# Kernel optimization log

Hardware: AMD Instinct MI355X
Metric: run time of the kernel (lower is better)

Reference implementation:

```python
import jax, jax.numpy as jnp
import numpy as np

N, E = 50000, 1600000
IN_DIM, HID, HEADS, DH, NCLS = 1280, 256, 4, 64, 6
NEG_SLOPE = 0.2
LN_EPS = 1e-5


def setup_inputs() -> dict:
    key = jax.random.key(0)
    ks = jax.random.split(key, 24)
    p = {}
    p['x'] = jax.random.normal(ks[0], (N, IN_DIM), dtype=jnp.float32)
    p['edge_index'] = jax.random.randint(ks[1], (2, E), 0, N, dtype=jnp.int64)
    s = 0.05
    p['W_in'] = jax.random.normal(ks[2], (IN_DIM, HID), dtype=jnp.float32) * s
    p['b_in'] = jnp.zeros((HID,), jnp.float32)
    for l in range(2):
        p[f'W_gat{l}'] = jax.random.normal(ks[3 + 6 * l], (HID, HEADS * DH), dtype=jnp.float32) * s
        p[f'att_src{l}'] = jax.random.normal(ks[4 + 6 * l], (HEADS, DH), dtype=jnp.float32) * s
        p[f'att_dst{l}'] = jax.random.normal(ks[5 + 6 * l], (HEADS, DH), dtype=jnp.float32) * s
        p[f'b_gat{l}'] = jnp.zeros((HEADS * DH,), jnp.float32)
        p[f'ln_g{l}'] = jnp.ones((HID,), jnp.float32)
        p[f'ln_b{l}'] = jnp.zeros((HID,), jnp.float32)
    p['W_c1'] = jax.random.normal(ks[20], (HID, HID // 2), dtype=jnp.float32) * s
    p['b_c1'] = jnp.zeros((HID // 2,), jnp.float32)
    p['W_c2'] = jax.random.normal(ks[21], (HID // 2, NCLS), dtype=jnp.float32) * s
    p['b_c2'] = jnp.zeros((NCLS,), jnp.float32)
    return p


def _layer_norm(h, g, b):
    mu = jnp.mean(h, axis=-1, keepdims=True)
    var = jnp.mean((h - mu) ** 2, axis=-1, keepdims=True)
    return (h - mu) * jax.lax.rsqrt(var + LN_EPS) * g + b


def _gat_conv(h, src, dst, W, a_src, a_dst, bias):
    # h: [N, HID] -> per-head projections [N, H, DH]
    xh = (h @ W).reshape(N, HEADS, DH)
    al_src = jnp.sum(xh * a_src, axis=-1)  # [N, H]
    al_dst = jnp.sum(xh * a_dst, axis=-1)  # [N, H]
    e = jax.nn.leaky_relu(al_src[src] + al_dst[dst], NEG_SLOPE)  # [E', H]
    # edge softmax over incoming edges of each destination node
    m = jax.ops.segment_max(e, dst, num_segments=N)
    e = jnp.exp(e - m[dst])
    denom = jax.ops.segment_sum(e, dst, num_segments=N)
    w = e / denom[dst]  # [E', H]
    msg = xh[src] * w[:, :, None]  # [E', H, DH]
    out = jax.ops.segment_sum(msg, dst, num_segments=N)  # [N, H, DH]
    return out.reshape(N, HEADS * DH) + bias


def reference(x, edge_index, W_in, b_in, W_gat0, att_src0, att_dst0, b_gat0, ln_g0, ln_b0,
              W_gat1, att_src1, att_dst1, b_gat1, ln_g1, ln_b1, W_c1, b_c1, W_c2, b_c2):
    # add self loops (PyG GATConv default)
    loop = jnp.arange(N, dtype=edge_index.dtype)
    src = jnp.concatenate([edge_index[0], loop])
    dst = jnp.concatenate([edge_index[1], loop])

    h = jax.nn.relu(x @ W_in + b_in)

    for (Wg, asrc, adst, bg, g, b) in ((W_gat0, att_src0, att_dst0, b_gat0, ln_g0, ln_b0),
                                       (W_gat1, att_src1, att_dst1, b_gat1, ln_g1, ln_b1)):
        h_new = _gat_conv(h, src, dst, Wg, asrc, adst, bg)
        h_new = jax.nn.relu(_layer_norm(h_new, g, b))
        h = h + h_new

    logits = jax.nn.relu(h @ W_c1 + b_c1) @ W_c2 + b_c2
    return logits
```

## Files before the change

kernel.cpp:

```cpp
#include <hip/hip_runtime.h>

#define NN 50000
#define EE 1600000
#define INDIM 1280
#define HID 256
#define HEADS 4
#define DHD 64
#define NCLS 6
#define NEG 0.2f
#define LNEPS 1e-5f

typedef __attribute__((ext_vector_type(8))) short short8;
typedef __attribute__((ext_vector_type(4))) float floatx4;

__device__ __forceinline__ unsigned short f2b(float f) {
    unsigned int u = __float_as_uint(f);
    u += 0x7FFF + ((u >> 16) & 1);
    return (unsigned short)(u >> 16);
}
__device__ __forceinline__ float b2f(unsigned short b) {
    return __uint_as_float(((unsigned int)b) << 16);
}

#define WAIT_LGKM0() __builtin_amdgcn_s_waitcnt(0xC07F)

__global__ void init_cnt_kernel(int* __restrict__ cnt) {
    int n = blockIdx.x * 256 + threadIdx.x;
    if (n < NN) cnt[n] = 1;
}

__global__ void count_edges_kernel(const int* __restrict__ dst, int* __restrict__ cnt) {
    int e = blockIdx.x * 256 + threadIdx.x;
    if (e < EE) atomicAdd(&cnt[dst[e]], 1);
}

__global__ __launch_bounds__(1024) void scan1_kernel(const int* __restrict__ cnt,
                                                     int* __restrict__ scanned,
                                                     int* __restrict__ chtot, int n) {
    __shared__ int wsum[16];
    int tid = threadIdx.x, lane = tid & 63, wv = tid >> 6;
    int i = blockIdx.x * 1024 + tid;
    int s = (i < n) ? cnt[i] : 0;
#pragma unroll
    for (int off = 1; off < 64; off <<= 1) {
        int t = __shfl_up(s, off, 64);
        if (lane >= off) s += t;
    }
    if (lane == 63) wsum[wv] = s;
    __syncthreads();
    if (tid < 16) {
        int ws = wsum[tid];
#pragma unroll
        for (int off = 1; off < 16; off <<= 1) {
            int t = __shfl_up(ws, off, 16);
            if (tid >= off) ws += t;
        }
        wsum[tid] = ws;
    }
    __syncthreads();
    s += (wv > 0) ? wsum[wv - 1] : 0;
    if (i < n) scanned[i] = s;
    if (tid == 1023) chtot[blockIdx.x] = s;
}

__global__ void scan2_kernel(int* __restrict__ chtot, int nch) {
    int lane = threadIdx.x;
    int v = (lane < nch) ? chtot[lane] : 0;
#pragma unroll
    for (int off = 1; off < 64; off <<= 1) {
        int t = __shfl_up(v, off, 64);
        if (lane >= off) v += t;
    }
    if (lane < nch) chtot[lane] = v;
}

__global__ void scan3_kernel(const int* __restrict__ scanned, const int* __restrict__ chtot,
                             int* __restrict__ rowptr, int n) {
    int i = blockIdx.x * 256 + threadIdx.x;
    if (i == 0) rowptr[0] = 0;
    if (i < n) {
        int ch = i >> 10;
        rowptr[i + 1] = scanned[i] + (ch ? chtot[ch - 1] : 0);
    }
}

__global__ void copyfill_kernel(const int* __restrict__ rowptr, int* __restrict__ cursor,
                                int* __restrict__ csr) {
    int n = blockIdx.x * 256 + threadIdx.x;
    if (n < NN) {
        int p = rowptr[n];
        csr[p] = n;
        cursor[n] = p + 1;
    }
}

__global__ void scatter_edges_kernel(const int* __restrict__ src, const int* __restrict__ dst,
                                     int* __restrict__ cursor, int* __restrict__ csr) {
    int e = blockIdx.x * 256 + threadIdx.x;
    if (e < EE) {
        int d = dst[e];
        int pos = atomicAdd(&cursor[d], 1);
        csr[pos] = src[e];
    }
}

__global__ void pack_w_kernel(const float* __restrict__ W, unsigned short* __restrict__ out,
                              int K, int N) {
    int idx = blockIdx.x * 256 + threadIdx.x;
    int total = (K >> 6) * (N >> 4) * 2 * 64;
    if (idx >= total) return;
    int ln = idx & 63;
    int t = idx >> 6;
    int ks = t & 1; t >>= 1;
    int NT = N >> 4;
    int nt = t % NT, kc = t / NT;
    int n = nt * 16 + (ln & 15);
    int k = kc * 64 + ks * 32 + ((ln >> 4) << 3);
    unsigned short u[8];
#pragma unroll
    for (int j = 0; j < 8; j++) u[j] = f2b(W[(size_t)(k + j) * N + n]);
    *(int4*)&out[(size_t)idx * 8] = *(const int4*)u;
}

__global__ __launch_bounds__(256) void inproj_kernel(const float* __restrict__ Af,
                                                     const unsigned short* __restrict__ Bf,
                                                     const float* __restrict__ bias,
                                                     float* __restrict__ Cf,
                                                     unsigned short* __restrict__ Cb) {
    constexpr int KI = 20;
    __shared__ __align__(16) unsigned short Als[2][8192];
    int tid = threadIdx.x, wv = tid >> 6, ln = tid & 63;
    int m0 = blockIdx.x * 128;

    int srow[4], scol[4];
#pragma unroll
    for (int i = 0; i < 4; i++) {
        int s = tid + i * 256;
        int r = s >> 3;
        srow[i] = min(m0 + r, NN - 1);
        scol[i] = ((s & 7) ^ (r & 7)) * 8;
    }

    floatx4 acc[8][4] = {};
    short8 breg[8];
    float4 af[8];

    auto issueA = [&](int k) {
#pragma unroll
        for (int i = 0; i < 4; i++) {
            const float* p = Af + (size_t)srow[i] * INDIM + k * 64 + scol[i];
            af[i * 2] = *(const float4*)p;
            af[i * 2 + 1] = *(const float4*)(p + 4);
        }
    };
    auto issueB = [&](int k) {
#pragma unroll
        for (int nw = 0; nw < 4; nw++)
#pragma unroll
            for (int ks = 0; ks < 2; ks++)
                breg[nw * 2 + ks] = *(const short8*)(
                    Bf + ((((size_t)k * 16 + (wv * 4 + nw)) * 2 + ks) * 64 + ln) * 8);
    };
    auto writeA = [&](int k) {
        unsigned short* dst = &Als[k & 1][0];
#pragma unroll
        for (int i = 0; i < 4; i++) {
            unsigned short u[8] = {f2b(af[2 * i].x), f2b(af[2 * i].y),
                                   f2b(af[2 * i].z), f2b(af[2 * i].w),
                                   f2b(af[2 * i + 1].x), f2b(af[2 * i + 1].y),
                                   f2b(af[2 * i + 1].z), f2b(af[2 * i + 1].w)};
            *(int4*)&dst[(tid + i * 256) * 8] = *(const int4*)u;
        }
    };
    auto compute = [&](int k) {
        const unsigned short* src = &Als[k & 1][0];
#pragma unroll
        for (int ks = 0; ks < 2; ks++) {
            short8 a[8];
#pragma unroll
            for (int mt = 0; mt < 8; mt++) {
                int row = mt * 16 + (ln & 15);
                int g = ks * 4 + (ln >> 4);
                a[mt] = *(const short8*)&src[row * 64 + (g ^ (row & 7)) * 8];
            }
#pragma unroll
            for (int nw = 0; nw < 4; nw++)
#pragma unroll
                for (int mt = 0; mt < 8; mt++)
                    acc[mt][nw] = __builtin_amdgcn_mfma_f32_16x16x32_bf16(
                        a[mt], breg[nw * 2 + ks], acc[mt][nw], 0, 0, 0);
        }
    };

    issueA(0);
    writeA(0);
    issueA(1);
    issueB(0);
    WAIT_LGKM0();
    __builtin_amdgcn_s_barrier();

    for (int k = 0; k < KI; k++) {
        compute(k);
        if (k + 1 < KI) {
            issueB(k + 1);
            writeA(k + 1);
        }
        if (k + 2 < KI) issueA(k + 2);
        if (k + 1 < KI) {
            WAIT_LGKM0();
            __builtin_amdgcn_s_barrier();
        }
    }

#pragma unroll
    for (int mt = 0; mt < 8; mt++) {
#pragma unroll
        for (int nw = 0; nw < 4; nw++) {
            int col = (wv * 4 + nw) * 16 + (ln & 15);
            int rb = m0 + mt * 16 + (ln >> 4) * 4;
            float bi = bias[col];
#pragma unroll
            for (int r = 0; r < 4; r++) {
                int row = rb + r;
                if (row < NN) {
                    float v = fmaxf(acc[mt][nw][r] + bi, 0.f);
                    Cf[(size_t)row * HID + col] = v;
                    Cb[(size_t)row * HID + col] = f2b(v);
                }
            }
        }
    }
}

template <int KI, int NT, int ACT, int WB16, int PROJ, int CLS>
__global__ __launch_bounds__(256) void pgemm_kernel(const unsigned short* __restrict__ Ab,
                                                    const unsigned short* __restrict__ Bf,
                                                    const float* __restrict__ bias,
                                                    unsigned short* __restrict__ Cb,
                                                    const float* __restrict__ aps,
                                                    const float* __restrict__ apd,
                                                    float* __restrict__ als,
                                                    float* __restrict__ ald,
                                                    const float* __restrict__ W2,
                                                    const float* __restrict__ b2,
                                                    float* __restrict__ out2,
                                                    int M) {
    constexpr int NW = NT / 4;
    constexpr int K = KI * 64;
    __shared__ __align__(16) unsigned short Als[2][4096];
    int tid = threadIdx.x, wv = tid >> 6, ln = tid & 63;
    int m0 = blockIdx.x * 64;

    int srow[2], scol[2];
#pragma unroll
    for (int i = 0; i < 2; i++) {
        int s = tid + i * 256;
        int r = s >> 3;
        srow[i] = min(m0 + r, M - 1);
        scol[i] = ((s & 7) ^ (r & 7)) * 8;
    }

    floatx4 acc[4][NW] = {};
    short8 breg[2][NW * 2];
    int4 ai0[2], ai1[2];

    auto issueA = [&](int k, int4* ai) {
#pragma unroll
        for (int i = 0; i < 2; i++)
            ai[i] = *(const int4*)(Ab + (size_t)srow[i] * K + k * 64 + scol[i]);
    };
    auto issueB = [&](int k, short8* b) {
#pragma unroll
        for (int nw = 0; nw < NW; nw++)
#pragma unroll
            for (int ks = 0; ks < 2; ks++)
                b[nw * 2 + ks] = *(const short8*)(
                    Bf + ((((size_t)k * NT + (wv * NW + nw)) * 2 + ks) * 64 + ln) * 8);
    };
    auto writeA = [&](int k, const int4* ai) {
        unsigned short* dst = &Als[k & 1][0];
#pragma unroll
        for (int i = 0; i < 2; i++) *(int4*)&dst[(tid + i * 256) * 8] = ai[i];
    };
    auto compute = [&](int k, const short8* b) {
        const unsigned short* src = &Als[k & 1][0];
#pragma unroll
        for (int ks = 0; ks < 2; ks++) {
            short8 a[4];
#pragma unroll
            for (int mt = 0; mt < 4; mt++) {
                int row = mt * 16 + (ln & 15);
                int g = ks * 4 + (ln >> 4);
                a[mt] = *(const short8*)&src[row * 64 + (g ^ (row & 7)) * 8];
            }
#pragma unroll
            for (int nw = 0; nw < NW; nw++)
#pragma unroll
                for (int mt = 0; mt < 4; mt++)
                    acc[mt][nw] = __builtin_amdgcn_mfma_f32_16x16x32_bf16(
                        a[mt], b[nw * 2 + ks], acc[mt][nw], 0, 0, 0);
        }
    };

    issueA(0, ai0);
    issueB(0, breg[0]);
    writeA(0, ai0);
    WAIT_LGKM0();
    __builtin_amdgcn_s_barrier();

#pragma unroll
    for (int kk = 0; kk < KI / 2; kk++) {
        int k = kk * 2;
        issueA(k + 1, ai1);
        issueB(k + 1, breg[1]);
        compute(k, breg[0]);
        writeA(k + 1, ai1);
        WAIT_LGKM0();
        __builtin_amdgcn_s_barrier();
        if (k + 2 < KI) {
            issueA(k + 2, ai0);
            issueB(k + 2, breg[0]);
        }
        compute(k + 1, breg[1]);
        if (k + 2 < KI) {
            writeA(k + 2, ai0);
            WAIT_LGKM0();
            __builtin_amdgcn_s_barrier();
        }
    }

    constexpr int Nout = NT * 16;
    if constexpr (WB16) {
#pragma unroll
        for (int mt = 0; mt < 4; mt++) {
#pragma unroll
            for (int nw = 0; nw < NW; nw++) {
                int col = (wv * NW + nw) * 16 + (ln & 15);
                int rb = m0 + mt * 16 + (ln >> 4) * 4;
                float bi = bias ? bias[col] : 0.f;
#pragma unroll
                for (int r = 0; r < 4; r++) {
                    int row = rb + r;
                    if (row < M) {
                        float v = acc[mt][nw][r] + bi;
                        if (ACT) v = fmaxf(v, 0.f);
                        Cb[(size_t)row * Nout + col] = f2b(v);
                    }
                }
            }
        }
    }

    if constexpr (PROJ) {
        float avs[NW], avd[NW];
#pragma unroll
        for (int nw = 0; nw < NW; nw++) {
            int d = nw * 16 + (ln & 15);
            avs[nw] = aps[wv * DHD + d];
            avd[nw] = apd[wv * DHD + d];
        }
#pragma unroll
        for (int mt = 0; mt < 4; mt++) {
#pragma unroll
            for (int r = 0; r < 4; r++) {
                float ssum = 0.f, dsum = 0.f;
#pragma unroll
                for (int nw = 0; nw < NW; nw++) {
                    float v = acc[mt][nw][r];
                    ssum = fmaf(v, avs[nw], ssum);
                    dsum = fmaf(v, avd[nw], dsum);
                }
#pragma unroll
                for (int m = 8; m > 0; m >>= 1) {
                    ssum += __shfl_xor(ssum, m, 16);
                    dsum += __shfl_xor(dsum, m, 16);
                }
                int row = m0 + mt * 16 + (ln >> 4) * 4 + r;
                if ((ln & 15) == 0 && row < M) {
                    als[row * 4 + wv] = ssum;
                    ald[row * 4 + wv] = dsum;
                }
            }
        }
    }

    if constexpr (CLS) {
        __shared__ float cred[64][4][NCLS];
        float w2[NW][NCLS];
#pragma unroll
        for (int nw = 0; nw < NW; nw++) {
            int col = (wv * NW + nw) * 16 + (ln & 15);
#pragma unroll
            for (int c = 0; c < NCLS; c++) w2[nw][c] = W2[col * NCLS + c];
        }
#pragma unroll
        for (int mt = 0; mt < 4; mt++) {
#pragma unroll
            for (int r = 0; r < 4; r++) {
                float p[NCLS] = {};
#pragma unroll
                for (int nw = 0; nw < NW; nw++) {
                    int col = (wv * NW + nw) * 16 + (ln & 15);
                    float v = fmaxf(acc[mt][nw][r] + bias[col], 0.f);
#pragma unroll
                    for (int c = 0; c < NCLS; c++) p[c] = fmaf(v, w2[nw][c], p[c]);
                }
#pragma unroll
                for (int m = 8; m > 0; m >>= 1)
#pragma unroll
                    for (int c = 0; c < NCLS; c++) p[c] += __shfl_xor(p[c], m, 16);
                int rl = mt * 16 + (ln >> 4) * 4 + r;
                if ((ln & 15) == 0)
#pragma unroll
                    for (int c = 0; c < NCLS; c++) cred[rl][wv][c] = p[c];
            }
        }
        __syncthreads();
        for (int t = tid; t < 64 * NCLS; t += 256) {
            int row = t / NCLS, c = t % NCLS;
            if (m0 + row < M) {
                float s = cred[row][0][c] + cred[row][1][c] + cred[row][2][c] +
                          cred[row][3][c] + b2[c];
                out2[(size_t)(m0 + row) * NCLS + c] = s;
            }
        }
    }
}

__global__ __launch_bounds__(256) void agg_ln_kernel(const int* __restrict__ rowptr,
                                                     const int* __restrict__ csr,
                                                     const float* __restrict__ al_s,
                                                     const float* __restrict__ al_d,
                                                     const unsigned short* __restrict__ xhb,
                                                     const float* __restrict__ bgat,
                                                     const float* __restrict__ g,
                                                     const float* __restrict__ bb,
                                                     float* __restrict__ h,
                                                     unsigned short* __restrict__ hb) {
    int wv = threadIdx.x >> 6, ln = threadIdx.x & 63;
    int n = blockIdx.x * 4 + wv;
    if (n >= NN) return;
    int start = rowptr[n], end = rowptr[n + 1];
    int half = ln >> 5;
    int j = ln & 31;
    int head = j >> 3;
    float adh = al_d[n * 4 + head];

    float p[8] = {}, q[8] = {};
    float dsp = 0.f, dsq = 0.f;

    int i = start + half;
    for (; i + 2 < end; i += 4) {
        int s0 = csr[i], s1 = csr[i + 2];
        float e0 = al_s[s0 * 4 + head] + adh; e0 = e0 > 0.f ? e0 : NEG * e0;
        float e1 = al_s[s1 * 4 + head] + adh; e1 = e1 > 0.f ? e1 : NEG * e1;
        float w0 = __expf(e0), w1 = __expf(e1);
        dsp += w0; dsq += w1;
        short8 u0 = *(const short8*)&xhb[(size_t)s0 * HID + j * 8];
        short8 u1 = *(const short8*)&xhb[(size_t)s1 * HID + j * 8];
#pragma unroll
        for (int k = 0; k < 8; k++) {
            p[k] = fmaf(w0, b2f((unsigned short)u0[k]), p[k]);
            q[k] = fmaf(w1, b2f((unsigned short)u1[k]), q[k]);
        }
    }
    if (i < end) {
        int s0 = csr[i];
        float e0 = al_s[s0 * 4 + head] + adh; e0 = e0 > 0.f ? e0 : NEG * e0;
        float w0 = __expf(e0);
        dsp += w0;
        short8 u0 = *(const short8*)&xhb[(size_t)s0 * HID + j * 8];
#pragma unroll
        for (int k = 0; k < 8; k++) p[k] = fmaf(w0, b2f((unsigned short)u0[k]), p[k]);
    }

    float ds = dsp + dsq;
    ds += __shfl_xor(ds, 32, 64);
    float inv = 1.f / ds;

    const float4* bgp = (const float4*)&bgat[j * 8];
    float4 bg0 = bgp[0], bg1 = bgp[1];
    float bgk[8] = {bg0.x, bg0.y, bg0.z, bg0.w, bg1.x, bg1.y, bg1.z, bg1.w};

    float vv[8];
    float ps = 0.f, ps2 = 0.f;
#pragma unroll
    for (int k = 0; k < 8; k++) {
        float t = p[k] + q[k];
        t += __shfl_xor(t, 32, 64);
        float val = t * inv + bgk[k];
        vv[k] = val;
        ps += val;
        ps2 = fmaf(val, val, ps2);
    }
#pragma unroll
    for (int off = 16; off > 0; off >>= 1) {
        ps += __shfl_xor(ps, off, 64);
        ps2 += __shfl_xor(ps2, off, 64);
    }
    float mu = ps * (1.f / HID);
    float var = ps2 * (1.f / HID) - mu * mu;
    float rs = rsqrtf(var + LNEPS);

    const float4* gp = (const float4*)&g[j * 8];
    const float4* bp = (const float4*)&bb[j * 8];
    float4 g0 = gp[0], g1 = gp[1];
    float4 c0 = bp[0], c1 = bp[1];
    float gk[8] = {g0.x, g0.y, g0.z, g0.w, g1.x, g1.y, g1.z, g1.w};
    float ck[8] = {c0.x, c0.y, c0.z, c0.w, c1.x, c1.y, c1.z, c1.w};

    size_t idx = (size_t)n * HID + j * 8;
    const float4* hp = (const float4*)&h[idx];
    float4 h0 = hp[0], h1 = hp[1];
    float hk[8] = {h0.x, h0.y, h0.z, h0.w, h1.x, h1.y, h1.z, h1.w};

    float nh[8];
#pragma unroll
    for (int k = 0; k < 8; k++) {
        float o = fmaxf((vv[k] - mu) * rs * gk[k] + ck[k], 0.f);
        nh[k] = hk[k] + o;
    }

    if (half == 0) {
        ((float4*)&h[idx])[0] = make_float4(nh[0], nh[1], nh[2], nh[3]);
        ((float4*)&h[idx])[1] = make_float4(nh[4], nh[5], nh[6], nh[7]);
    } else {
        unsigned short ub[8];
#pragma unroll
        for (int k = 0; k < 8; k++) ub[k] = f2b(nh[k]);
        *(int4*)&hb[idx] = *(const int4*)ub;
    }
}

extern "C" void kernel_launch(void* const* d_in, const int* in_sizes, int n_in,
                              void* d_out, int out_size, void* d_ws, size_t ws_size,
                              hipStream_t stream) {
    const float* x    = (const float*)d_in[0];
    const int*   ei   = (const int*)d_in[1];
    const float* W_in = (const float*)d_in[2];
    const float* b_in = (const float*)d_in[3];
    const float* W_gat[2]   = {(const float*)d_in[4],  (const float*)d_in[10]};
    const float* att_src[2] = {(const float*)d_in[5],  (const float*)d_in[11]};
    const float* att_dst[2] = {(const float*)d_in[6],  (const float*)d_in[12]};
    const float* b_gat[2]   = {(const float*)d_in[7],  (const float*)d_in[13]};
    const float* ln_g[2]    = {(const float*)d_in[8],  (const float*)d_in[14]};
    const float* ln_b[2]    = {(const float*)d_in[9],  (const float*)d_in[15]};
    const float* W_c1 = (const float*)d_in[16];
    const float* b_c1 = (const float*)d_in[17];
    const float* W_c2 = (const float*)d_in[18];
    const float* b_c2 = (const float*)d_in[19];

    char* ws = (char*)d_ws;
    size_t off = 0;
    auto alloc = [&](size_t bytes) -> void* {
        void* p = ws + off;
        off += (bytes + 255) & ~(size_t)255;
        return p;
    };
    float*          h   = (float*)alloc((size_t)NN * HID * 4);
    unsigned short* hb  = (unsigned short*)alloc((size_t)NN * HID * 2);
    unsigned short* xhb = (unsigned short*)alloc((size_t)NN * HID * 2);
    float* al_s = (float*)alloc((size_t)NN * HEADS * 4);
    float* al_d = (float*)alloc((size_t)NN * HEADS * 4);
    int* rowptr  = (int*)alloc((size_t)(NN + 1) * 4);
    int* cursor  = (int*)alloc((size_t)NN * 4);
    int* csr     = (int*)alloc((size_t)(EE + NN) * 4);
    int* scanned = (int*)alloc((size_t)NN * 4);
    int* chtot   = (int*)alloc(64 * 4);
    unsigned short* WinF = (unsigned short*)alloc((size_t)HID * INDIM * 2);
    unsigned short* WgF0 = (unsigned short*)alloc((size_t)HID * HID * 2);
    unsigned short* WgF1 = (unsigned short*)alloc((size_t)HID * HID * 2);
    unsigned short* Wc1F = (unsigned short*)alloc((size_t)(HID / 2) * HID * 2);
    unsigned short* WgF[2] = {WgF0, WgF1};

    const int* srcv = ei;
    const int* dstv = ei + EE;

    pack_w_kernel<<<(INDIM * HID / 8 + 255) / 256, 256, 0, stream>>>(W_in, WinF, INDIM, HID);
    pack_w_kernel<<<(HID * HID / 8 + 255) / 256, 256, 0, stream>>>(W_gat[0], WgF0, HID, HID);
    pack_w_kernel<<<(HID * HID / 8 + 255) / 256, 256, 0, stream>>>(W_gat[1], WgF1, HID, HID);
    pack_w_kernel<<<(HID * (HID / 2) / 8 + 255) / 256, 256, 0, stream>>>(W_c1, Wc1F, HID, HID / 2);

    int nch = (NN + 1023) / 1024;
    init_cnt_kernel<<<(NN + 255) / 256, 256, 0, stream>>>(cursor);
    count_edges_kernel<<<(EE + 255) / 256, 256, 0, stream>>>(dstv, cursor);
    scan1_kernel<<<nch, 1024, 0, stream>>>(cursor, scanned, chtot, NN);
    scan2_kernel<<<1, 64, 0, stream>>>(chtot, nch);
    scan3_kernel<<<(NN + 255) / 256, 256, 0, stream>>>(scanned, chtot, rowptr, NN);
    copyfill_kernel<<<(NN + 255) / 256, 256, 0, stream>>>(rowptr, cursor, csr);
    scatter_edges_kernel<<<(EE + 255) / 256, 256, 0, stream>>>(srcv, dstv, cursor, csr);

    inproj_kernel<<<(NN + 127) / 128, 256, 0, stream>>>(x, WinF, b_in, h, hb);

    int MB64 = (NN + 63) / 64;
    for (int l = 0; l < 2; l++) {
        pgemm_kernel<4, 16, 0, 1, 1, 0><<<MB64, 256, 0, stream>>>(
            hb, WgF[l], nullptr, xhb,
            att_src[l], att_dst[l], al_s, al_d, nullptr, nullptr, nullptr, NN);
        agg_ln_kernel<<<(NN + 3) / 4, 256, 0, stream>>>(rowptr, csr, al_s, al_d, xhb,
                                                        b_gat[l], ln_g[l], ln_b[l], h, hb);
    }

    pgemm_kernel<4, 8, 1, 0, 0, 1><<<MB64, 256, 0, stream>>>(
        hb, Wc1F, b_c1, nullptr,
        nullptr, nullptr, nullptr, nullptr, W_c2, b_c2, (float*)d_out, NN);
}
```

Baseline: 991.8 us.

## Rewrite input projection with direct global-to-LDS loads and triple buffering

The input projection GEMM now uses global_load_lds to stream fp32 A tiles and bf16 B tiles directly into a triple-buffered LDS ring, synchronised with vmcnt waits. The fp32 to bf16 conversion moves to read time with v_cvt_pk_bf16_f32. The M tile shrinks from 128 to 64 rows, the K step from 64 to 32, and W_in is repacked into a matching per-32 layout. This removes the register staging and VALU conversion path on the load side and aims to raise occupancy and overlap. The cost is more blocks, more B traffic per row, and more barriers per K.

Result: no change. 998.0 us (+0.6%).

```diff
diff --git a/kernel.cpp b/kernel.cpp
--- a/kernel.cpp
+++ b/kernel.cpp
@@ -23,6 +23,12 @@
 }
 
 #define WAIT_LGKM0() __builtin_amdgcn_s_waitcnt(0xC07F)
+#define VMCNT6() asm volatile("s_waitcnt vmcnt(6)" ::: "memory")
+#define VMCNT0() asm volatile("s_waitcnt vmcnt(0)" ::: "memory")
+
+typedef const __attribute__((address_space(1))) unsigned int g_u32;
+typedef __attribute__((address_space(3))) unsigned int l_u32;
+#define GLOAD16(gp, lp) __builtin_amdgcn_global_load_lds((g_u32*)(gp), (l_u32*)(lp), 16, 0, 0)
 
 __global__ void init_cnt_kernel(int* __restrict__ cnt) {
     int n = blockIdx.x * 256 + threadIdx.x;
@@ -122,98 +128,96 @@
     *(int4*)&out[(size_t)idx * 8] = *(const int4*)u;
 }
 
+__global__ void pack_w32_kernel(const float* __restrict__ W, unsigned short* __restrict__ out) {
+    int idx = blockIdx.x * 256 + threadIdx.x;
+    if (idx >= 40 * 16 * 64) return;
+    int ln = idx & 63;
+    int t = idx >> 6;
+    int nt = t & 15;
+    int s = t >> 4;
+    int n = nt * 16 + (ln & 15);
+    int k = s * 32 + ((ln >> 4) << 3);
+    unsigned short u[8];
+#pragma unroll
+    for (int j = 0; j < 8; j++) u[j] = f2b(W[(size_t)(k + j) * HID + n]);
+    *(int4*)&out[(size_t)idx * 8] = *(const int4*)u;
+}
+
 __global__ __launch_bounds__(256) void inproj_kernel(const float* __restrict__ Af,
-                                                     const unsigned short* __restrict__ Bf,
+                                                     const unsigned short* __restrict__ B32,
                                                      const float* __restrict__ bias,
                                                      float* __restrict__ Cf,
                                                      unsigned short* __restrict__ Cb) {
-    constexpr int KI = 20;
-    __shared__ __align__(16) unsigned short Als[2][8192];
+    constexpr int KS = 40;
+    constexpr int ABYTES = 8192;
+    constexpr int BBYTES = 16384;
+    constexpr int SBYTES = ABYTES + BBYTES;
+    __shared__ __align__(16) char lds[3 * SBYTES];
     int tid = threadIdx.x, wv = tid >> 6, ln = tid & 63;
-    int m0 = blockIdx.x * 128;
-
-    int srow[4], scol[4];
-#pragma unroll
-    for (int i = 0; i < 4; i++) {
-        int s = tid + i * 256;
-        int r = s >> 3;
-        srow[i] = min(m0 + r, NN - 1);
-        scol[i] = ((s & 7) ^ (r & 7)) * 8;
-    }
-
-    floatx4 acc[8][4] = {};
-    short8 breg[8];
-    float4 af[8];
-
-    auto issueA = [&](int k) {
-#pragma unroll
-        for (int i = 0; i < 4; i++) {
-            const float* p = Af + (size_t)srow[i] * INDIM + k * 64 + scol[i];
-            af[i * 2] = *(const float4*)p;
-            af[i * 2 + 1] = *(const float4*)(p + 4);
-        }
+    int m0 = blockIdx.x * 64;
+
+    int arow0 = wv * 16 + (ln >> 3);
+    int arow1 = arow0 + 8;
+    int acb = ((ln & 7) * 16) ^ (((ln >> 3) & 7) << 4);
+    const char* asrc0 = (const char*)(Af + (size_t)min(m0 + arow0, NN - 1) * INDIM) + acb;
+    const char* asrc1 = (const char*)(Af + (size_t)min(m0 + arow1, NN - 1) * INDIM) + acb;
+    const char* bsrc = (const char*)B32 + wv * 4096 + ln * 16;
+
+    int aslot = wv * 2048 + ln * 16;
+    int bslot = wv * 4096 + ln * 16;
+
+    auto issue = [&](int k) {
+        char* a = &lds[(k % 3) * SBYTES];
+        char* b = a + ABYTES;
+        GLOAD16(asrc0 + (size_t)k * 128, a + aslot);
+        GLOAD16(asrc1 + (size_t)k * 128, a + aslot + 1024);
+        const char* bs = bsrc + (size_t)k * BBYTES;
+        GLOAD16(bs, b + bslot);
+        GLOAD16(bs + 1024, b + bslot + 1024);
+        GLOAD16(bs + 2048, b + bslot + 2048);
+        GLOAD16(bs + 3072, b + bslot + 3072);
     };
-    auto issueB = [&](int k) {
+
+    floatx4 acc[4][4] = {};
+    int g32 = (ln >> 4) * 32;
+
+    issue(0);
+    issue(1);
+
+    for (int k = 0; k < KS; k++) {
+        if (k == KS - 1) VMCNT0(); else VMCNT6();
+        __builtin_amdgcn_s_barrier();
+        asm volatile("" ::: "memory");
+        if (k + 2 < KS) issue(k + 2);
+
+        const char* a = &lds[(k % 3) * SBYTES];
+        const char* b = a + ABYTES;
+        short8 bfrag[4];
 #pragma unroll
         for (int nw = 0; nw < 4; nw++)
-#pragma unroll
-            for (int ks = 0; ks < 2; ks++)
-                breg[nw * 2 + ks] = *(const short8*)(
-                    Bf + ((((size_t)k * 16 + (wv * 4 + nw)) * 2 + ks) * 64 + ln) * 8);
-    };
-    auto writeA = [&](int k) {
-        unsigned short* dst = &Als[k & 1][0];
-#pragma unroll
-        for (int i = 0; i < 4; i++) {
-            unsigned short u[8] = {f2b(af[2 * i].x), f2b(af[2 * i].y),
-                                   f2b(af[2 * i].z), f2b(af[2 * i].w),
-                                   f2b(af[2 * i + 1].x), f2b(af[2 * i + 1].y),
-                                   f2b(af[2 * i + 1].z), f2b(af[2 * i + 1].w)};
-            *(int4*)&dst[(tid + i * 256) * 8] = *(const int4*)u;
-        }
-    };
-    auto compute = [&](int k) {
-        const unsigned short* src = &Als[k & 1][0];
-#pragma unroll
-        for (int ks = 0; ks < 2; ks++) {
-            short8 a[8];
-#pragma unroll
-            for (int mt = 0; mt < 8; mt++) {
-                int row = mt * 16 + (ln & 15);
-                int g = ks * 4 + (ln >> 4);
-                a[mt] = *(const short8*)&src[row * 64 + (g ^ (row & 7)) * 8];
-            }
+            bfrag[nw] = *(const short8*)(b + (((wv * 4 + nw) * 64 + ln) << 4));
+#pragma unroll
+        for (int mt = 0; mt < 4; mt++) {
+            int row = mt * 16 + (ln & 15);
+            int base = row * 128;
+            int sw = (row & 7) << 4;
+            float4 f0 = *(const float4*)(a + base + (g32 ^ sw));
+            float4 f1 = *(const float4*)(a + base + ((g32 + 16) ^ sw));
+            union { int4 i; short8 s; } u;
+            asm("v_cvt_pk_bf16_f32 %0, %1, %2" : "=v"(u.i.x) : "v"(f0.x), "v"(f0.y));
+            asm("v_cvt_pk_bf16_f32 %0, %1, %2" : "=v"(u.i.y) : "v"(f0.z), "v"(f0.w));
+            asm("v_cvt_pk_bf16_f32 %0, %1, %2" : "=v"(u.i.z) : "v"(f1.x), "v"(f1.y));
+            asm("v_cvt_pk_bf16_f32 %0, %1, %2" : "=v"(u.i.w) : "v"(f1.z), "v"(f1.w));
 #pragma unroll
             for (int nw = 0; nw < 4; nw++)
-#pragma unroll
-                for (int mt = 0; mt < 8; mt++)
-                    acc[mt][nw] = __builtin_amdgcn_mfma_f32_16x16x32_bf16(
-                        a[mt], breg[nw * 2 + ks], acc[mt][nw], 0, 0, 0);
-        }
-    };
-
-    issueA(0);
-    writeA(0);
-    issueA(1);
-    issueB(0);
-    WAIT_LGKM0();
-    __builtin_amdgcn_s_barrier();
-
-    for (int k = 0; k < KI; k++) {
-        compute(k);
-        if (k + 1 < KI) {
-            issueB(k + 1);
-            writeA(k + 1);
-        }
-        if (k + 2 < KI) issueA(k + 2);
-        if (k + 1 < KI) {
-            WAIT_LGKM0();
-            __builtin_amdgcn_s_barrier();
-        }
-    }
-
-#pragma unroll
-    for (int mt = 0; mt < 8; mt++) {
+                acc[mt][nw] = __builtin_amdgcn_mfma_f32_16x16x32_bf16(
+                    u.s, bfrag[nw], acc[mt][nw], 0, 0, 0);
+        }
+        asm volatile("" ::: "memory");
+    }
+
+#pragma unroll
+    for (int mt = 0; mt < 4; mt++) {
 #pragma unroll
         for (int nw = 0; nw < 4; nw++) {
             int col = (wv * 4 + nw) * 16 + (ln & 15);
@@ -567,7 +571,7 @@
     int* csr     = (int*)alloc((size_t)(EE + NN) * 4);
     int* scanned = (int*)alloc((size_t)NN * 4);
     int* chtot   = (int*)alloc(64 * 4);
-    unsigned short* WinF = (unsigned short*)alloc((size_t)HID * INDIM * 2);
+    unsigned short* Win32 = (unsigned short*)alloc((size_t)HID * INDIM * 2);
     unsigned short* WgF0 = (unsigned short*)alloc((size_t)HID * HID * 2);
     unsigned short* WgF1 = (unsigned short*)alloc((size_t)HID * HID * 2);
     unsigned short* Wc1F = (unsigned short*)alloc((size_t)(HID / 2) * HID * 2);
@@ -576,7 +580,7 @@
     const int* srcv = ei;
     const int* dstv = ei + EE;
 
-    pack_w_kernel<<<(INDIM * HID / 8 + 255) / 256, 256, 0, stream>>>(W_in, WinF, INDIM, HID);
+    pack_w32_kernel<<<(40 * 16 * 64 + 255) / 256, 256, 0, stream>>>(W_in, Win32);
     pack_w_kernel<<<(HID * HID / 8 + 255) / 256, 256, 0, stream>>>(W_gat[0], WgF0, HID, HID);
     pack_w_kernel<<<(HID * HID / 8 + 255) / 256, 256, 0, stream>>>(W_gat[1], WgF1, HID, HID);
     pack_w_kernel<<<(HID * (HID / 2) / 8 + 255) / 256, 256, 0, stream>>>(W_c1, Wc1F, HID, HID / 2);
@@ -590,7 +594,7 @@
     copyfill_kernel<<<(NN + 255) / 256, 256, 0, stream>>>(rowptr, cursor, csr);
     scatter_edges_kernel<<<(EE + 255) / 256, 256, 0, stream>>>(srcv, dstv, cursor, csr);
 
-    inproj_kernel<<<(NN + 127) / 128, 256, 0, stream>>>(x, WinF, b_in, h, hb);
+    inproj_kernel<<<(NN + 63) / 64, 256, 0, stream>>>(x, Win32, b_in, h, hb);
 
     int MB64 = (NN + 63) / 64;
     for (int l = 0; l < 2; l++) {
```
